# Optimization experiments

Hardware: AMD Instinct MI355X
Metric: run time of the kernel (lower is better)

## Reference

```python
import jax, jax.numpy as jnp
import numpy as np

C = 1024
HEADS = 8
HD = C // HEADS
SF = 2
EPS = 1e-6
N, D, H, W = 2, 32, 40, 32


def _ln(x, w, b):
    m = jnp.mean(x, -1, keepdims=True)
    v = jnp.mean((x - m) ** 2, -1, keepdims=True)
    return (x - m) * jax.lax.rsqrt(v + EPS) * w + b


def _mlp2(x, w1, b1, w2, b2):
    # Linear -> exact GELU -> Linear (matches nn.Sequential(Linear, GELU, Linear))
    return jax.nn.gelu(x @ w1.T + b1, approximate=False) @ w2.T + b2


def setup_inputs() -> dict:
    key = jax.random.key(0)
    ks = jax.random.split(key, 24)
    p = lambda i, shape: jax.random.normal(ks[i], shape, jnp.float32) * 0.02
    return {
        "x": jax.random.normal(ks[0], (N, D, H, W, C), jnp.float32),
        "q_w": p(1, (C, C)),
        "k_w1": p(2, (C, C)), "k_b1": p(3, (C,)),
        "k_w2": p(4, (C, C)), "k_b2": p(5, (C,)),
        "v_w1": p(6, (C, C)), "v_b1": p(7, (C,)),
        "v_w2": p(8, (C, C)), "v_b2": p(9, (C,)),
        "lnq_w": jnp.ones((C,), jnp.float32), "lnq_b": jnp.zeros((C,), jnp.float32),
        "lnk_w": jnp.ones((C,), jnp.float32), "lnk_b": jnp.zeros((C,), jnp.float32),
        "lnv_w": jnp.ones((C,), jnp.float32), "lnv_b": jnp.zeros((C,), jnp.float32),
        "in_w": p(10, (3 * C, C)), "in_b": p(11, (3 * C,)),
        "out_w": p(12, (C, C)), "out_b": p(13, (C,)),
        "mlp_w1": p(14, (2 * C, C)), "mlp_b1": p(15, (2 * C,)),
        "mlp_w2": p(16, (2 * C, 2 * C)), "mlp_b2": p(17, (2 * C,)),
    }


def reference(x, q_w, k_w1, k_b1, k_w2, k_b2, v_w1, v_b1, v_w2, v_b2,
              lnq_w, lnq_b, lnk_w, lnk_b, lnv_w, lnv_b,
              in_w, in_b, out_w, out_b, mlp_w1, mlp_b1, mlp_w2, mlp_b2):
    n, d, h, w, c = x.shape
    dg, hg, wg = d // SF, h // SF, w // SF
    cube = SF ** 3

    x_flat = x.reshape(n, -1, c)                      # [N, T, C], T = D*H*W
    k = _ln(_mlp2(x_flat, k_w1, k_b1, k_w2, k_b2), lnk_w, lnk_b)
    v = _ln(_mlp2(x_flat, v_w1, v_b1, v_w2, v_b2), lnv_w, lnv_b)

    # Trilinear downsample by exactly 2 (align_corners=False) == 2x2x2 mean pool.
    q = x.reshape(n, dg, SF, hg, SF, wg, SF, c).mean(axis=(2, 4, 6))
    q = q.reshape(n, -1, c)                            # [N, Q, C]
    query = _ln(q @ q_w.T, lnq_w, lnq_b)               # q_proj_1 has no bias

    def regions(t):
        t = t.reshape(n, dg, SF, hg, SF, wg, SF, c)
        t = t.transpose(0, 1, 3, 5, 2, 4, 6, 7)
        return t.reshape(n, dg * hg * wg, cube, c)     # [N, Q, 8, C]

    k_r = regions(k)
    v_r = regions(v)

    wq, wk, wv = in_w[:C], in_w[C:2 * C], in_w[2 * C:]
    bq, bk, bv = in_b[:C], in_b[C:2 * C], in_b[2 * C:]
    qh = (query @ wq.T + bq).reshape(n, -1, HEADS, HD)           # [N,Q,h,hd]
    kh = (k_r @ wk.T + bk).reshape(n, -1, cube, HEADS, HD)       # [N,Q,8,h,hd]
    vh = (v_r @ wv.T + bv).reshape(n, -1, cube, HEADS, HD)

    scale = 1.0 / np.sqrt(HD).astype(np.float32)
    scores = jnp.einsum('nqhd,nqkhd->nqhk', qh, kh) * scale
    attn = jax.nn.softmax(scores, axis=-1)
    o = jnp.einsum('nqhk,nqkhd->nqhd', attn, vh).reshape(n, -1, c)
    o = o @ out_w.T + out_b                            # MHA out_proj

    o = _mlp2(o, mlp_w1, mlp_b1, mlp_w2, mlp_b2)       # [N, Q, 2C]
    return o.reshape(n, dg, hg, wg, 2 * c)
```

## Files before the change

kernel.cpp:

```cpp
#include <hip/hip_runtime.h>

typedef __attribute__((ext_vector_type(8))) short bf16x8;
typedef __attribute__((ext_vector_type(4))) float f32x4;
typedef unsigned short u16;

__device__ inline u16 f2b(float f) {
  union { float f; unsigned u; } x; x.f = f;
  unsigned r = x.u + 0x7FFFu + ((x.u >> 16) & 1u);
  return (u16)(r >> 16);
}
__device__ inline float b2f(u16 s) {
  union { unsigned u; float f; } x; x.u = ((unsigned)s) << 16;
  return x.f;
}
__device__ inline float gelu_f(float v) {
  return 0.5f * v * (1.0f + erff(v * 0.70710678118654752f));
}
__device__ inline void gll16(const void* g, void* lds) {
  __builtin_amdgcn_global_load_lds((const __attribute__((address_space(1))) void*)g,
                                   (__attribute__((address_space(3))) void*)lds,
                                   16, 0, 0);
}

__global__ __launch_bounds__(256) void cvt_w(const float* __restrict__ s,
                                             u16* __restrict__ d, int n4) {
  int i = blockIdx.x * 256 + threadIdx.x;
  if (i < n4) {
    float4 v = ((const float4*)s)[i];
    ushort4 o; o.x = f2b(v.x); o.y = f2b(v.y); o.z = f2b(v.z); o.w = f2b(v.w);
    ((ushort4*)d)[i] = o;
  }
}

__global__ __launch_bounds__(256) void cat_bias(const float* __restrict__ a,
                                                const float* __restrict__ b,
                                                float* __restrict__ o) {
  int i = blockIdx.x * 256 + threadIdx.x;
  if (i < 1024) { o[i] = a[i]; o[1024 + i] = b[i]; }
}

__global__ __launch_bounds__(256) void pool_cvt(const float* __restrict__ xg,
                                                u16* __restrict__ Xb,
                                                u16* __restrict__ Qp) {
  int qr = blockIdx.x;
  int wgi = qr & 15;
  int hgi = (qr >> 4) % 20;
  int dgi = qr / 320;
  int c = threadIdx.x * 4;
  float sx = 0.f, sy = 0.f, sz = 0.f, sw = 0.f;
#pragma unroll
  for (int j = 0; j < 8; ++j) {
    int tr = ((2 * dgi + (j >> 2)) * 40 + (2 * hgi + ((j >> 1) & 1))) * 32 +
             (2 * wgi + (j & 1));
    long off = (long)tr * 1024 + c;
    float4 v = *(const float4*)&xg[off];
    ushort4 o; o.x = f2b(v.x); o.y = f2b(v.y); o.z = f2b(v.z); o.w = f2b(v.w);
    *(ushort4*)&Xb[off] = o;
    sx += v.x; sy += v.y; sz += v.z; sw += v.w;
  }
  ushort4 o;
  o.x = f2b(sx * 0.125f); o.y = f2b(sy * 0.125f);
  o.z = f2b(sz * 0.125f); o.w = f2b(sw * 0.125f);
  *(ushort4*)&Qp[(long)qr * 1024 + c] = o;
}

__global__ __launch_bounds__(256) void ln_ip(u16* __restrict__ X,
                                             const float* __restrict__ w,
                                             const float* __restrict__ b) {
  long row = blockIdx.x;
  int c = threadIdx.x * 4;
  ushort4 v = *(const ushort4*)&X[row * 1024 + c];
  float f0 = b2f(v.x), f1 = b2f(v.y), f2 = b2f(v.z), f3 = b2f(v.w);
  float s = f0 + f1 + f2 + f3;
  float q = f0 * f0 + f1 * f1 + f2 * f2 + f3 * f3;
#pragma unroll
  for (int off = 32; off >= 1; off >>= 1) {
    s += __shfl_xor(s, off);
    q += __shfl_xor(q, off);
  }
  __shared__ float red[8];
  int wv = threadIdx.x >> 6, ln = threadIdx.x & 63;
  if (ln == 0) { red[wv] = s; red[4 + wv] = q; }
  __syncthreads();
  s = red[0] + red[1] + red[2] + red[3];
  q = red[4] + red[5] + red[6] + red[7];
  float mean = s * (1.f / 1024.f);
  float var = q * (1.f / 1024.f) - mean * mean;
  float rs = rsqrtf(var + 1e-6f);
  float4 wv4 = *(const float4*)&w[c];
  float4 bv4 = *(const float4*)&b[c];
  ushort4 o;
  o.x = f2b((f0 - mean) * rs * wv4.x + bv4.x);
  o.y = f2b((f1 - mean) * rs * wv4.y + bv4.y);
  o.z = f2b((f2 - mean) * rs * wv4.z + bv4.z);
  o.w = f2b((f3 - mean) * rs * wv4.w + bv4.w);
  *(ushort4*)&X[row * 1024 + c] = o;
}

#define BK 32
template <int EPI>
__global__ __launch_bounds__(256) void gemm_bt(const u16* __restrict__ A,
                                               const u16* __restrict__ B,
                                               const float* __restrict__ bias,
                                               float* __restrict__ Cf,
                                               u16* __restrict__ Cb,
                                               int M, int N, int K, int lda,
                                               int nbx, int nby) {
  __shared__ __align__(16) u16 As0[128 * BK];
  __shared__ __align__(16) u16 Bs0[128 * BK];
  __shared__ __align__(16) u16 As1[128 * BK];
  __shared__ __align__(16) u16 Bs1[128 * BK];
  const int tid = threadIdx.x;

  int L = blockIdx.x, bx, by;
  if ((nbx & 7) == 0) {
    int xcd = L & 7, j = L >> 3, ppx = nbx >> 3;
    int pj = j / nby;
    bx = xcd * ppx + pj;
    by = j - pj * nby;
  } else {
    bx = L % nbx;
    by = L / nbx;
  }
  const int bm = bx * 128, bn = by * 128;

  const int l = tid & 63, wv = tid >> 6;
  const int wm = (wv >> 1) * 64, wn = (wv & 1) * 64;
  const int lr = l & 15, kg = l >> 4;

  const int ea = tid * 8, eb = (256 + tid) * 8;
  const int ra = ea >> 5, ca = ea & 31;
  const int rb = eb >> 5, cbn = eb & 31;
  int gra = bm + ra; if (gra > M - 1) gra = M - 1;
  int grb = bm + rb; if (grb > M - 1) grb = M - 1;
  const u16* pa0 = A + (long)gra * lda + ca;
  const u16* pa1 = A + (long)grb * lda + cbn;
  const u16* pb0 = B + (long)(bn + ra) * K + ca;
  const u16* pb1 = B + (long)(bn + rb) * K + cbn;

  f32x4 acc[4][4] = {};
  const int nt = K / BK;

#define STAGE(AS, BS, k0)                \
  do {                                   \
    gll16(pa0 + (k0), &(AS)[ea]);        \
    gll16(pb0 + (k0), &(BS)[ea]);        \
    gll16(pa1 + (k0), &(AS)[eb]);        \
    gll16(pb1 + (k0), &(BS)[eb]);        \
  } while (0)

#define COMPUTE(AS, BS)                                                       \
  do {                                                                        \
    bf16x8 af[4], bfr[4];                                                     \
    _Pragma("unroll") for (int m = 0; m < 4; ++m)                             \
        af[m] = *(const bf16x8*)&(AS)[(wm + m * 16 + lr) * BK + kg * 8];      \
    _Pragma("unroll") for (int n = 0; n < 4; ++n)                             \
        bfr[n] = *(const bf16x8*)&(BS)[(wn + n * 16 + lr) * BK + kg * 8];     \
    _Pragma("unroll") for (int m = 0; m < 4; ++m)                             \
        _Pragma("unroll") for (int n = 0; n < 4; ++n)                         \
            acc[m][n] = __builtin_amdgcn_mfma_f32_16x16x32_bf16(              \
                af[m], bfr[n], acc[m][n], 0, 0, 0);                           \
  } while (0)

  STAGE(As0, Bs0, 0);
  __syncthreads();
  for (int t = 0; t < nt; t += 2) {
    if (t + 1 < nt) STAGE(As1, Bs1, (t + 1) * BK);
    COMPUTE(As0, Bs0);
    __syncthreads();
    if (t + 2 < nt) STAGE(As0, Bs0, (t + 2) * BK);
    COMPUTE(As1, Bs1);
    __syncthreads();
  }
#undef STAGE
#undef COMPUTE

#pragma unroll
  for (int m = 0; m < 4; ++m) {
    int row0 = bm + wm + m * 16 + kg * 4;
#pragma unroll
    for (int n = 0; n < 4; ++n) {
      int col = bn + wn + n * 16 + lr;
      float bsv = (EPI == 3) ? 0.f : bias[col];
#pragma unroll
      for (int r = 0; r < 4; ++r) {
        int row = row0 + r;
        if (row < M) {
          float v = acc[m][n][r] + bsv;
          if (EPI == 1) v = gelu_f(v);
          if (EPI == 2) Cf[(long)row * N + col] = v;
          else Cb[(long)row * N + col] = f2b(v);
        }
      }
    }
  }
}

__global__ __launch_bounds__(256) void attn_k(const u16* __restrict__ QH,
                                              const u16* __restrict__ KH,
                                              const u16* __restrict__ VH,
                                              u16* __restrict__ O) {
  int qr = blockIdx.x;
  int wgi = qr & 15;
  int hgi = (qr >> 4) % 20;
  int dgi = qr / 320;
  int c0 = (threadIdx.x >> 5) * 128 + (threadIdx.x & 31) * 4;
  ushort4 qv = *(const ushort4*)&QH[(long)qr * 1024 + c0];
  float q0 = b2f(qv.x), q1 = b2f(qv.y), q2 = b2f(qv.z), q3 = b2f(qv.w);
  long trs[8];
  float sc[8];
#pragma unroll
  for (int j = 0; j < 8; ++j) {
    int tr = ((2 * dgi + (j >> 2)) * 40 + (2 * hgi + ((j >> 1) & 1))) * 32 +
             (2 * wgi + (j & 1));
    trs[j] = (long)tr * 1024 + c0;
    ushort4 kv = *(const ushort4*)&KH[trs[j]];
    float p = q0 * b2f(kv.x) + q1 * b2f(kv.y) + q2 * b2f(kv.z) + q3 * b2f(kv.w);
    p += __shfl_xor(p, 16); p += __shfl_xor(p, 8); p += __shfl_xor(p, 4);
    p += __shfl_xor(p, 2);  p += __shfl_xor(p, 1);
    sc[j] = p * 0.088388347648318447f;
  }
  float mx = sc[0];
#pragma unroll
  for (int j = 1; j < 8; ++j) mx = fmaxf(mx, sc[j]);
  float ssum = 0.f;
#pragma unroll
  for (int j = 0; j < 8; ++j) { sc[j] = expf(sc[j] - mx); ssum += sc[j]; }
  float inv = 1.0f / ssum;
  float o0 = 0, o1 = 0, o2 = 0, o3 = 0;
#pragma unroll
  for (int j = 0; j < 8; ++j) {
    ushort4 vv = *(const ushort4*)&VH[trs[j]];
    float p = sc[j] * inv;
    o0 += p * b2f(vv.x); o1 += p * b2f(vv.y);
    o2 += p * b2f(vv.z); o3 += p * b2f(vv.w);
  }
  ushort4 ov; ov.x = f2b(o0); ov.y = f2b(o1); ov.z = f2b(o2); ov.w = f2b(o3);
  *(ushort4*)&O[(long)qr * 1024 + c0] = ov;
}

extern "C" void kernel_launch(void* const* d_in, const int* in_sizes, int n_in,
                              void* d_out, int out_size, void* d_ws,
                              size_t ws_size, hipStream_t stream) {
  const float* x      = (const float*)d_in[0];
  const float* q_w    = (const float*)d_in[1];
  const float* k_w1   = (const float*)d_in[2];
  const float* k_b1   = (const float*)d_in[3];
  const float* k_w2   = (const float*)d_in[4];
  const float* k_b2   = (const float*)d_in[5];
  const float* v_w1   = (const float*)d_in[6];
  const float* v_b1   = (const float*)d_in[7];
  const float* v_w2   = (const float*)d_in[8];
  const float* v_b2   = (const float*)d_in[9];
  const float* lnq_w  = (const float*)d_in[10];
  const float* lnq_b  = (const float*)d_in[11];
  const float* lnk_w  = (const float*)d_in[12];
  const float* lnk_b  = (const float*)d_in[13];
  const float* lnv_w  = (const float*)d_in[14];
  const float* lnv_b  = (const float*)d_in[15];
  const float* in_w   = (const float*)d_in[16];
  const float* in_b   = (const float*)d_in[17];
  const float* out_w  = (const float*)d_in[18];
  const float* out_b  = (const float*)d_in[19];
  const float* mlp_w1 = (const float*)d_in[20];
  const float* mlp_b1 = (const float*)d_in[21];
  const float* mlp_w2 = (const float*)d_in[22];
  const float* mlp_b2 = (const float*)d_in[23];
  float* out = (float*)d_out;

  char* base = (char*)d_ws;
  size_t off = 0;
  auto alloc_us = [&](size_t elems) -> u16* {
    u16* r = (u16*)(base + off);
    off += ((elems * 2 + 255) & ~(size_t)255);
    return r;
  };
  const size_t CC = 1024 * 1024;
  u16* wb_q   = alloc_us(CC);
  u16* wb_kv1 = alloc_us(2 * CC);
  u16* wb_k2  = alloc_us(CC);
  u16* wb_v2  = alloc_us(CC);
  u16* wb_in  = alloc_us(3 * CC);
  u16* wb_out = alloc_us(CC);
  u16* wb_m1  = alloc_us(2 * CC);
  u16* wb_m2  = alloc_us(4 * CC);
  float* b_kv1 = (float*)(base + off); off += 2048 * 4;

  auto cvt = [&](const float* s, u16* d, size_t n) {
    int n4 = (int)(n / 4);
    cvt_w<<<(n4 + 255) / 256, 256, 0, stream>>>(s, d, n4);
  };
  cvt(q_w, wb_q, CC);
  cvt(k_w1, wb_kv1, CC);        cvt(v_w1, wb_kv1 + CC, CC);
  cvt(k_w2, wb_k2, CC);         cvt(v_w2, wb_v2, CC);
  cvt(in_w, wb_in, 3 * CC);     cvt(out_w, wb_out, CC);
  cvt(mlp_w1, wb_m1, 2 * CC);   cvt(mlp_w2, wb_m2, 4 * CC);
  cat_bias<<<4, 256, 0, stream>>>(k_b1, v_b1, b_kv1);

  int s = 16;
  for (int cand = 1; cand <= 16; cand <<= 1) {
    size_t Tc_ = 40960ull / cand;
    size_t need = off + Tc_ * 11520ull + (1ull << 20);
    if (need <= ws_size) { s = cand; break; }
  }
  const int dcount = 32 / s;
  const int dgc = dcount / 2;
  const int Tc = dcount * 1280;
  const int Tq = dgc * 320;

  u16* Xb  = alloc_us((size_t)Tc * 1024);
  u16* Hb2 = alloc_us((size_t)Tc * 2048);
  u16* Kb  = alloc_us((size_t)Tc * 1024);
  u16* Vb  = alloc_us((size_t)Tc * 1024);
  u16* Qp  = alloc_us((size_t)Tq * 1024);
  u16* QQ  = alloc_us((size_t)Tq * 1024);
  u16* QHb = alloc_us((size_t)Tq * 1024);
  u16* Ob  = alloc_us((size_t)Tq * 1024);
  u16* O2  = alloc_us((size_t)Tq * 1024);
  u16* Hm  = Kb;

  auto launch_gemm = [&](int EPI, const u16* A, const u16* B, const float* bias,
                         float* Cf, u16* Cb, int M, int N, int K, int lda) {
    int nbx = (M + 127) / 128, nby = N / 128;
    dim3 g(nbx * nby);
    switch (EPI) {
      case 0: gemm_bt<0><<<g, 256, 0, stream>>>(A, B, bias, Cf, Cb, M, N, K, lda, nbx, nby); break;
      case 1: gemm_bt<1><<<g, 256, 0, stream>>>(A, B, bias, Cf, Cb, M, N, K, lda, nbx, nby); break;
      case 2: gemm_bt<2><<<g, 256, 0, stream>>>(A, B, bias, Cf, Cb, M, N, K, lda, nbx, nby); break;
      default: gemm_bt<3><<<g, 256, 0, stream>>>(A, B, bias, Cf, Cb, M, N, K, lda, nbx, nby); break;
    }
  };

  for (int n = 0; n < 2; ++n) {
    for (int sl = 0; sl < s; ++sl) {
      long tok0 = (long)n * 40960 + (long)sl * dcount * 1280;
      long q0g  = (long)n * 5120 + (long)sl * dgc * 320;
      const float* xg = x + tok0 * 1024;

      pool_cvt<<<Tq, 256, 0, stream>>>(xg, Xb, Qp);

      launch_gemm(1, Xb, wb_kv1, b_kv1, nullptr, Hb2, Tc, 2048, 1024, 1024);
      launch_gemm(0, Hb2, wb_k2, k_b2, nullptr, Kb, Tc, 1024, 1024, 2048);
      ln_ip<<<Tc, 256, 0, stream>>>(Kb, lnk_w, lnk_b);
      launch_gemm(0, Hb2 + 1024, wb_v2, v_b2, nullptr, Vb, Tc, 1024, 1024, 2048);
      ln_ip<<<Tc, 256, 0, stream>>>(Vb, lnv_w, lnv_b);

      launch_gemm(3, Qp, wb_q, nullptr, nullptr, QQ, Tq, 1024, 1024, 1024);
      ln_ip<<<Tq, 256, 0, stream>>>(QQ, lnq_w, lnq_b);
      launch_gemm(0, QQ, wb_in, in_b, nullptr, QHb, Tq, 1024, 1024, 1024);

      launch_gemm(0, Kb, wb_in + CC, in_b + 1024, nullptr, Xb, Tc, 1024, 1024, 1024);
      launch_gemm(0, Vb, wb_in + 2 * CC, in_b + 2048, nullptr, Hb2, Tc, 1024, 1024, 1024);

      attn_k<<<Tq, 256, 0, stream>>>(QHb, Xb, Hb2, Ob);

      launch_gemm(0, Ob, wb_out, out_b, nullptr, O2, Tq, 1024, 1024, 1024);
      launch_gemm(1, O2, wb_m1, mlp_b1, nullptr, Hm, Tq, 2048, 1024, 1024);
      launch_gemm(2, Hm, wb_m2, mlp_b2, out + q0g * 2048, nullptr, Tq, 2048, 2048, 2048);
    }
  }
}
```

Measured before the change: 2.314 ms.

## Batch independent GEMMs into grouped launches and merge per-batch chunk loop

```diff
diff --git a/kernel.cpp b/kernel.cpp
--- a/kernel.cpp
+++ b/kernel.cpp
@@ -97,15 +97,55 @@
   *(ushort4*)&X[row * 1024 + c] = o;
 }
 
+__global__ __launch_bounds__(256) void ln2_ip(u16* X1, const float* w1,
+                                              const float* b1, u16* X2,
+                                              const float* w2, const float* b2,
+                                              long rows1) {
+  long row = blockIdx.x;
+  u16* X = X1; const float* w = w1; const float* b = b1;
+  if (row >= rows1) { X = X2; w = w2; b = b2; row -= rows1; }
+  int c = threadIdx.x * 4;
+  ushort4 v = *(const ushort4*)&X[row * 1024 + c];
+  float f0 = b2f(v.x), f1 = b2f(v.y), f2 = b2f(v.z), f3 = b2f(v.w);
+  float s = f0 + f1 + f2 + f3;
+  float q = f0 * f0 + f1 * f1 + f2 * f2 + f3 * f3;
+#pragma unroll
+  for (int off = 32; off >= 1; off >>= 1) {
+    s += __shfl_xor(s, off);
+    q += __shfl_xor(q, off);
+  }
+  __shared__ float red[8];
+  int wv = threadIdx.x >> 6, ln = threadIdx.x & 63;
+  if (ln == 0) { red[wv] = s; red[4 + wv] = q; }
+  __syncthreads();
+  s = red[0] + red[1] + red[2] + red[3];
+  q = red[4] + red[5] + red[6] + red[7];
+  float mean = s * (1.f / 1024.f);
+  float var = q * (1.f / 1024.f) - mean * mean;
+  float rs = rsqrtf(var + 1e-6f);
+  float4 wv4 = *(const float4*)&w[c];
+  float4 bv4 = *(const float4*)&b[c];
+  ushort4 o;
+  o.x = f2b((f0 - mean) * rs * wv4.x + bv4.x);
+  o.y = f2b((f1 - mean) * rs * wv4.y + bv4.y);
+  o.z = f2b((f2 - mean) * rs * wv4.z + bv4.z);
+  o.w = f2b((f3 - mean) * rs * wv4.w + bv4.w);
+  *(ushort4*)&X[row * 1024 + c] = o;
+}
+
+#define MFMA16(a, b, c) __builtin_amdgcn_mfma_f32_16x16x32_bf16((a), (b), (c), 0, 0, 0)
+
 #define BK 32
 template <int EPI>
-__global__ __launch_bounds__(256) void gemm_bt(const u16* __restrict__ A,
-                                               const u16* __restrict__ B,
-                                               const float* __restrict__ bias,
-                                               float* __restrict__ Cf,
-                                               u16* __restrict__ Cb,
-                                               int M, int N, int K, int lda,
-                                               int nbx, int nby) {
+__global__ __launch_bounds__(256) void gemm_bt(const u16* A, const u16* B,
+                                               const float* bias,
+                                               float* __restrict__ Cf, u16* Cb,
+                                               int M1, int N, int K, int lda,
+                                               int nbx, int nby,
+                                               const u16* A2, const u16* B2,
+                                               const float* bias2, u16* Cb2, int M2,
+                                               const u16* A3, const u16* B3,
+                                               const float* bias3, u16* Cb3, int M3) {
   __shared__ __align__(16) u16 As0[128 * BK];
   __shared__ __align__(16) u16 Bs0[128 * BK];
   __shared__ __align__(16) u16 As1[128 * BK];
@@ -122,7 +162,14 @@
     bx = L % nbx;
     by = L / nbx;
   }
-  const int bm = bx * 128, bn = by * 128;
+  int bm = bx * 128;
+  const int bn = by * 128;
+
+  int M = M1;
+  if (bm >= M1) {
+    if (bm < M1 + M2) { A = A2; B = B2; bias = bias2; Cb = Cb2; bm -= M1; M = M2; }
+    else { A = A3; B = B3; bias = bias3; Cb = Cb3; bm -= (M1 + M2); M = M3; }
+  }
 
   const int l = tid & 63, wv = tid >> 6;
   const int wm = (wv >> 1) * 64, wn = (wv & 1) * 64;
@@ -158,8 +205,7 @@
         bfr[n] = *(const bf16x8*)&(BS)[(wn + n * 16 + lr) * BK + kg * 8];     \
     _Pragma("unroll") for (int m = 0; m < 4; ++m)                             \
         _Pragma("unroll") for (int n = 0; n < 4; ++n)                         \
-            acc[m][n] = __builtin_amdgcn_mfma_f32_16x16x32_bf16(              \
-                af[m], bfr[n], acc[m][n], 0, 0, 0);                           \
+            acc[m][n] = MFMA16(af[m], bfr[n], acc[m][n]);                     \
   } while (0)
 
   STAGE(As0, Bs0, 0);
@@ -297,15 +343,12 @@
   cvt(mlp_w1, wb_m1, 2 * CC);   cvt(mlp_w2, wb_m2, 4 * CC);
   cat_bias<<<4, 256, 0, stream>>>(k_b1, v_b1, b_kv1);
 
-  int s = 16;
-  for (int cand = 1; cand <= 16; cand <<= 1) {
-    size_t Tc_ = 40960ull / cand;
-    size_t need = off + Tc_ * 11520ull + (1ull << 20);
-    if (need <= ws_size) { s = cand; break; }
-  }
-  const int dcount = 32 / s;
-  const int dgc = dcount / 2;
-  const int Tc = dcount * 1280;
+  int dgc = 1;
+  for (int cand = 32; cand >= 1; cand >>= 1) {
+    size_t Tc_ = (size_t)cand * 2560;
+    if (off + Tc_ * 11520ull + (1ull << 20) <= ws_size) { dgc = cand; break; }
+  }
+  const int Tc = dgc * 2560;
   const int Tq = dgc * 320;
 
   u16* Xb  = alloc_us((size_t)Tc * 1024);
@@ -319,44 +362,52 @@
   u16* O2  = alloc_us((size_t)Tq * 1024);
   u16* Hm  = Kb;
 
-  auto launch_gemm = [&](int EPI, const u16* A, const u16* B, const float* bias,
-                         float* Cf, u16* Cb, int M, int N, int K, int lda) {
-    int nbx = (M + 127) / 128, nby = N / 128;
+  auto launch = [&](int EPI, int N, int K, int lda,
+                    const u16* A1, const u16* B1, const float* s1, u16* C1, int M1,
+                    const u16* A2, const u16* B2, const float* s2, u16* C2, int M2,
+                    const u16* A3, const u16* B3, const float* s3, u16* C3, int M3,
+                    float* Cf) {
+    int nbx = (M1 + M2 + M3) / 128, nby = N / 128;
     dim3 g(nbx * nby);
     switch (EPI) {
-      case 0: gemm_bt<0><<<g, 256, 0, stream>>>(A, B, bias, Cf, Cb, M, N, K, lda, nbx, nby); break;
-      case 1: gemm_bt<1><<<g, 256, 0, stream>>>(A, B, bias, Cf, Cb, M, N, K, lda, nbx, nby); break;
-      case 2: gemm_bt<2><<<g, 256, 0, stream>>>(A, B, bias, Cf, Cb, M, N, K, lda, nbx, nby); break;
-      default: gemm_bt<3><<<g, 256, 0, stream>>>(A, B, bias, Cf, Cb, M, N, K, lda, nbx, nby); break;
+      case 0: gemm_bt<0><<<g, 256, 0, stream>>>(A1, B1, s1, Cf, C1, M1, N, K, lda, nbx, nby, A2, B2, s2, C2, M2, A3, B3, s3, C3, M3); break;
+      case 1: gemm_bt<1><<<g, 256, 0, stream>>>(A1, B1, s1, Cf, C1, M1, N, K, lda, nbx, nby, A2, B2, s2, C2, M2, A3, B3, s3, C3, M3); break;
+      case 2: gemm_bt<2><<<g, 256, 0, stream>>>(A1, B1, s1, Cf, C1, M1, N, K, lda, nbx, nby, A2, B2, s2, C2, M2, A3, B3, s3, C3, M3); break;
+      default: gemm_bt<3><<<g, 256, 0, stream>>>(A1, B1, s1, Cf, C1, M1, N, K, lda, nbx, nby, A2, B2, s2, C2, M2, A3, B3, s3, C3, M3); break;
     }
   };
-
-  for (int n = 0; n < 2; ++n) {
-    for (int sl = 0; sl < s; ++sl) {
-      long tok0 = (long)n * 40960 + (long)sl * dcount * 1280;
-      long q0g  = (long)n * 5120 + (long)sl * dgc * 320;
-      const float* xg = x + tok0 * 1024;
-
-      pool_cvt<<<Tq, 256, 0, stream>>>(xg, Xb, Qp);
-
-      launch_gemm(1, Xb, wb_kv1, b_kv1, nullptr, Hb2, Tc, 2048, 1024, 1024);
-      launch_gemm(0, Hb2, wb_k2, k_b2, nullptr, Kb, Tc, 1024, 1024, 2048);
-      ln_ip<<<Tc, 256, 0, stream>>>(Kb, lnk_w, lnk_b);
-      launch_gemm(0, Hb2 + 1024, wb_v2, v_b2, nullptr, Vb, Tc, 1024, 1024, 2048);
-      ln_ip<<<Tc, 256, 0, stream>>>(Vb, lnv_w, lnv_b);
-
-      launch_gemm(3, Qp, wb_q, nullptr, nullptr, QQ, Tq, 1024, 1024, 1024);
-      ln_ip<<<Tq, 256, 0, stream>>>(QQ, lnq_w, lnq_b);
-      launch_gemm(0, QQ, wb_in, in_b, nullptr, QHb, Tq, 1024, 1024, 1024);
-
-      launch_gemm(0, Kb, wb_in + CC, in_b + 1024, nullptr, Xb, Tc, 1024, 1024, 1024);
-      launch_gemm(0, Vb, wb_in + 2 * CC, in_b + 2048, nullptr, Hb2, Tc, 1024, 1024, 1024);
-
-      attn_k<<<Tq, 256, 0, stream>>>(QHb, Xb, Hb2, Ob);
-
-      launch_gemm(0, Ob, wb_out, out_b, nullptr, O2, Tq, 1024, 1024, 1024);
-      launch_gemm(1, O2, wb_m1, mlp_b1, nullptr, Hm, Tq, 2048, 1024, 1024);
-      launch_gemm(2, Hm, wb_m2, mlp_b2, out + q0g * 2048, nullptr, Tq, 2048, 2048, 2048);
-    }
-  }
-}
+  const u16* Z = nullptr;
+
+  for (int dg0 = 0; dg0 < 32; dg0 += dgc) {
+    const float* xg = x + (size_t)dg0 * 2560 * 1024;
+    long q0g = (long)dg0 * 320;
+
+    pool_cvt<<<Tq, 256, 0, stream>>>(xg, Xb, Qp);
+
+    launch(1, 2048, 1024, 1024, Xb, wb_kv1, b_kv1, Hb2, Tc,
+           Z, Z, nullptr, nullptr, 0, Z, Z, nullptr, nullptr, 0, nullptr);
+
+    launch(0, 1024, 1024, 2048, Hb2, wb_k2, k_b2, Kb, Tc,
+           Hb2 + 1024, wb_v2, v_b2, Vb, Tc, Z, Z, nullptr, nullptr, 0, nullptr);
+
+    ln2_ip<<<2 * Tc, 256, 0, stream>>>(Kb, lnk_w, lnk_b, Vb, lnv_w, lnv_b, Tc);
+
+    launch(3, 1024, 1024, 1024, Qp, wb_q, nullptr, QQ, Tq,
+           Z, Z, nullptr, nullptr, 0, Z, Z, nullptr, nullptr, 0, nullptr);
+    ln_ip<<<Tq, 256, 0, stream>>>(QQ, lnq_w, lnq_b);
+
+    launch(0, 1024, 1024, 1024, Kb, wb_in + CC, in_b + 1024, Xb, Tc,
+           Vb, wb_in + 2 * CC, in_b + 2048, Hb2, Tc,
+           QQ, wb_in, in_b, QHb, Tq, nullptr);
+
+    attn_k<<<Tq, 256, 0, stream>>>(QHb, Xb, Hb2, Ob);
+
+    launch(0, 1024, 1024, 1024, Ob, wb_out, out_b, O2, Tq,
+           Z, Z, nullptr, nullptr, 0, Z, Z, nullptr, nullptr, 0, nullptr);
+    launch(1, 2048, 1024, 1024, O2, wb_m1, mlp_b1, Hm, Tq,
+           Z, Z, nullptr, nullptr, 0, Z, Z, nullptr, nullptr, 0, nullptr);
+    launch(2, 2048, 2048, 2048, Hm, wb_m2, mlp_b2, nullptr, Tq,
+           Z, Z, nullptr, nullptr, 0, Z, Z, nullptr, nullptr, 0,
+           out + q0g * 2048);
+  }
+}
```

Result: no change. 2.310 ms (-0.2%).
